# Kernel optimization log

Hardware: AMD Instinct MI355X
Metric: run time of the kernel (lower is better)

The kernel has to match this reference:

```python
import jax, jax.numpy as jnp
import numpy as np

EPS = 1e-5

def _bn(x, g, b):
    # BatchNorm1d, training mode: batch stats over node dim, biased variance
    mu = jnp.mean(x, axis=0)
    var = jnp.mean((x - mu) ** 2, axis=0)
    return (x - mu) * jax.lax.rsqrt(var + EPS) * g + b

def _relconv_msg(h, Vl, ce, src):
    # basis-decomposed per-edge messages: m_e = sum_b ce[e,b] * (h[src_e] @ V_b)
    # scan over bases to avoid [E,B,f] intermediate
    E = src.shape[0]
    f = Vl.shape[-1]
    def step(m, xs):
        Vb, cb = xs  # [d,f], [E]
        return m + cb[:, None] * (h @ Vb)[src], None
    m0 = jnp.zeros((E, f), h.dtype)
    m, _ = jax.lax.scan(step, m0, (Vl, ce.T))
    return m

def setup_inputs() -> dict:
    key = jax.random.key(0)
    ks = jax.random.split(key, 12)
    N, E, d, R, B, L = 20000, 320000, 256, 64, 30, 3
    s = 0.05
    return {
        "h": jax.random.normal(ks[0], (N, d), jnp.float32),
        "norm": jax.random.uniform(ks[1], (E, 1), jnp.float32),
        "V": jax.random.normal(ks[2], (L, B, d, d), jnp.float32) * s,
        "comp": jax.random.normal(ks[3], (L, R, B), jnp.float32) * s,
        "bias": jax.random.normal(ks[4], (L, d), jnp.float32) * s,
        "W1": jax.random.normal(ks[5], (L, d, d), jnp.float32) * s,
        "b1": jax.random.normal(ks[6], (L, d), jnp.float32) * s,
        "g1": jnp.ones((L, d), jnp.float32),
        "bt1": jnp.zeros((L, d), jnp.float32),
        "W2": jax.random.normal(ks[7], (L, d, d), jnp.float32) * s,
        "b2": jax.random.normal(ks[8], (L, d), jnp.float32) * s,
        "g2": jnp.ones((L, d), jnp.float32),
        "bt2": jnp.zeros((L, d), jnp.float32),
        "src": jax.random.randint(ks[9], (E,), 0, N, jnp.int32),
        "dst": jax.random.randint(ks[10], (E,), 0, N, jnp.int32),
        "etypes": jax.random.randint(ks[11], (E,), 0, R, jnp.int32),
    }

def reference(h, norm, V, comp, bias, W1, b1, g1, bt1, W2, b2, g2, bt2, src, dst, etypes):
    N = h.shape[0]
    L = V.shape[0]
    reps = [h]
    for l in range(L):
        ce = comp[l][etypes]                    # [E,B] per-edge basis coeffs
        m = _relconv_msg(h, V[l], ce, src)      # [E,f]
        m = m * norm
        agg = jax.ops.segment_sum(m, dst, num_segments=N)  # scatter-sum to dst
        x = agg + bias[l]
        # MLP activation (2 layers): Linear -> BN -> ReLU -> Linear
        x1 = jax.nn.relu(_bn(x @ W1[l] + b1[l], g1[l], bt1[l]))
        x = x1 @ W2[l] + b2[l]
        # outer BatchNorm + ReLU (RGIN layer)
        h = jax.nn.relu(_bn(x, g2[l], bt2[l]))
        reps.append(h)
    return jnp.stack(reps)  # [L+1, N, d] hidden_rep
```

## Files before the change

### kernel.cpp

```cpp
#include <hip/hip_runtime.h>
#include <hip/hip_bf16.h>
#include <stdint.h>

#define DF   256
#define NBAS 30
#define RREL 64
#define NLAY 3
#define EPSBN 1e-5f

typedef short  bf16x8 __attribute__((ext_vector_type(8)));
typedef float  f32x4  __attribute__((ext_vector_type(4)));
typedef ushort u16x4  __attribute__((ext_vector_type(4)));

typedef __attribute__((address_space(1))) const unsigned int gu32;
typedef __attribute__((address_space(3))) unsigned int       lu32;

__device__ __forceinline__ void gload16(const void* g, void* l){
  __builtin_amdgcn_global_load_lds((gu32*)g, (lu32*)l, 16, 0, 0);
}

__device__ __forceinline__ ushort f2bf(float f){
  union { float f; uint32_t u; } v; v.f = f;
  uint32_t r = (v.u + 0x7FFFu + ((v.u >> 16) & 1u)) >> 16;
  return (ushort)r;
}
__device__ __forceinline__ float bf2f(ushort u){
  union { uint32_t u; float f; } v; v.u = (uint32_t)u << 16;
  return v.f;
}

__global__ __launch_bounds__(256) void k_hist_rel(const int* __restrict__ et,
                                                  int* __restrict__ counts, int E){
  __shared__ int lh[RREL];
  int t = threadIdx.x;
  if (t < RREL) lh[t] = 0;
  __syncthreads();
  int i = blockIdx.x*256 + t;
  if (i < E) atomicAdd(&lh[et[i]], 1);
  __syncthreads();
  if (t < RREL && lh[t]) atomicAdd(&counts[t], lh[t]);
}

__global__ void k_hist_dst(const int* __restrict__ dst, int* __restrict__ counts, int E){
  int i = blockIdx.x*blockDim.x + threadIdx.x;
  if (i < E) atomicAdd(&counts[dst[i]], 1);
}

__global__ void k_scan_rel(const int* __restrict__ counts,
                           int* __restrict__ relOff, int* __restrict__ tileOff){
  int l = threadIdx.x;
  int c  = counts[l];
  int tt = (c + 127) >> 7;
  int ic = c, it = tt;
  #pragma unroll
  for (int o = 1; o < 64; o <<= 1){
    int u = __shfl_up(ic, o); if (l >= o) ic += u;
    int v = __shfl_up(it, o); if (l >= o) it += v;
  }
  if (l == 0){ relOff[0] = 0; tileOff[0] = 0; }
  relOff[l+1]  = ic;
  tileOff[l+1] = it;
}

__global__ void k_scan_dst(const int* __restrict__ counts, int* __restrict__ offs, int n){
  __shared__ int tmp[1024];
  __shared__ int carry;
  int t = threadIdx.x;
  if (t == 0) carry = 0;
  __syncthreads();
  for (int s = 0; s < n; s += 1024){
    int i = s + t;
    int v = (i < n) ? counts[i] : 0;
    tmp[t] = v;
    __syncthreads();
    for (int o = 1; o < 1024; o <<= 1){
      int u = (t >= o) ? tmp[t - o] : 0;
      __syncthreads();
      tmp[t] += u;
      __syncthreads();
    }
    int incl = tmp[t];
    int base = carry;
    if (i < n) offs[i] = base + incl - v;
    __syncthreads();
    if (t == 1023) carry = base + incl;
    __syncthreads();
  }
  if (t == 0) offs[n] = carry;
}

__global__ __launch_bounds__(256) void k_place_rel(const int* __restrict__ et,
    const int* __restrict__ src, const int* __restrict__ relOff,
    int* __restrict__ cursor, int* __restrict__ srcR, int* __restrict__ posR, int E){
  __shared__ int lcnt[RREL];
  __shared__ int lbase[RREL];
  int t = threadIdx.x;
  if (t < RREL) lcnt[t] = 0;
  __syncthreads();
  int i = blockIdx.x*256 + t;
  int r = 0, my = 0;
  bool v = (i < E);
  if (v){ r = et[i]; my = atomicAdd(&lcnt[r], 1); }
  __syncthreads();
  if (t < RREL && lcnt[t]) lbase[t] = atomicAdd(&cursor[t], lcnt[t]);
  __syncthreads();
  if (v){
    int p = relOff[r] + lbase[r] + my;
    srcR[p] = src[i];
    posR[i] = p;
  }
}

__global__ __launch_bounds__(256) void k_place_dst(const int* __restrict__ dst,
    const int* __restrict__ offsD, int* __restrict__ cursorD,
    const int* __restrict__ posR, const float* __restrict__ nrm,
    int* __restrict__ dstPos, float* __restrict__ nrmD, int E){
  int i = blockIdx.x*256 + threadIdx.x;
  if (i < E){
    int d = dst[i];
    int q = offsD[d] + atomicAdd(&cursorD[d], 1);
    dstPos[posR[i]] = q;
    nrmD[q] = nrm[i];
  }
}

__global__ __launch_bounds__(256) void k_wrel(const float* __restrict__ V,
    const float* __restrict__ comp, ushort* __restrict__ Wt){
  const int r  = blockIdx.x;
  const int k0 = blockIdx.y*32;
  const int l  = blockIdx.z;
  const int col = threadIdx.x;
  float acc[32];
  #pragma unroll
  for (int kk = 0; kk < 32; ++kk) acc[kk] = 0.f;
  for (int b = 0; b < NBAS; ++b){
    float cb = comp[(size_t)(l*RREL + r)*NBAS + b];
    const float* Vb = V + (((size_t)(l*NBAS + b)*DF) + k0)*DF + col;
    #pragma unroll
    for (int kk = 0; kk < 32; ++kk) acc[kk] = fmaf(cb, Vb[(size_t)kk*DF], acc[kk]);
  }
  ushort* o = Wt + ((size_t)(l*RREL + r)*DF + col)*DF + k0;
  #pragma unroll
  for (int i4 = 0; i4 < 8; ++i4){
    u16x4 p;
    #pragma unroll
    for (int j = 0; j < 4; ++j) p[j] = f2bf(acc[i4*4 + j]);
    *(u16x4*)(o + i4*4) = p;
  }
}

__global__ void k_transpose_bf16(const float* __restrict__ in, ushort* __restrict__ out, int K){
  const float* inz  = in  + (size_t)blockIdx.z*K*DF;
  ushort*      outz = out + (size_t)blockIdx.z*DF*K;
  __shared__ float tile[32][33];
  int k0 = blockIdx.x*32, n0 = blockIdx.y*32;
  int tx = threadIdx.x & 31, ty = threadIdx.x >> 5;
  #pragma unroll
  for (int i = 0; i < 32; i += 8)
    tile[ty+i][tx] = inz[(size_t)(k0+ty+i)*DF + n0 + tx];
  __syncthreads();
  #pragma unroll
  for (int i = 0; i < 32; i += 8)
    outz[(size_t)(n0+ty+i)*K + k0 + tx] = f2bf(tile[tx][ty+i]);
}

__global__ __launch_bounds__(256) void k_f2b(const float* __restrict__ in,
                                             ushort* __restrict__ o){
  size_t i = ((size_t)blockIdx.x*256 + threadIdx.x)*4;
  f32x4 v = *(const f32x4*)(in + i);
  u16x4 p;
  #pragma unroll
  for (int j = 0; j < 4; ++j) p[j] = f2bf(v[j]);
  *(u16x4*)(o + i) = p;
}

__global__ __launch_bounds__(512) void k_edge_gemm(
    const ushort* __restrict__ xh, const ushort* __restrict__ Wt,
    const int* __restrict__ srcR, const int* __restrict__ dstPos,
    const int* __restrict__ relOff, const int* __restrict__ tileOff,
    ushort* __restrict__ mD){
  __shared__ __align__(16) ushort As[128*64];
  __shared__ __align__(16) ushort Bs[256*64];
  const int b = blockIdx.x;
  if (b >= tileOff[RREL]) return;
  int r = 0;
  #pragma unroll
  for (int step = 32; step; step >>= 1)
    if (r + step <= RREL-1 && tileOff[r + step] <= b) r += step;
  const int eb   = relOff[r] + (b - tileOff[r])*128;
  const int emax = relOff[r+1] - 1;
  const int rows = min(128, relOff[r+1] - eb);

  const int tid  = threadIdx.x;
  const int lane = tid & 63, wid = tid >> 6;
  const int wr = (wid >> 2)*64, wc = (wid & 3)*64;
  const int l15 = lane & 15, lhi = lane >> 4;
  const int ko = (tid & 7)*8;

  const ushort* pa[2];
  #pragma unroll
  for (int i = 0; i < 2; ++i){
    int e = eb + ((tid + i*512) >> 3);
    if (e > emax) e = emax;
    pa[i] = xh + (size_t)srcR[e]*DF + ko;
  }
  const ushort* Bt = Wt + (size_t)r*DF*DF;
  const ushort* pb[4];
  #pragma unroll
  for (int i = 0; i < 4; ++i)
    pb[i] = Bt + (size_t)((tid >> 3) + i*64)*DF + ko;

  const f32x4 z = {0.f, 0.f, 0.f, 0.f};
  f32x4 acc[4][4];
  #pragma unroll
  for (int m = 0; m < 4; ++m)
    #pragma unroll
    for (int n = 0; n < 4; ++n) acc[m][n] = z;

  for (int kt = 0; kt < 4; ++kt){
    const int kbase = kt*64;
    __syncthreads();
    #pragma unroll
    for (int i = 0; i < 2; ++i) gload16(pa[i] + kbase, As + (tid + i*512)*8);
    #pragma unroll
    for (int i = 0; i < 4; ++i) gload16(pb[i] + kbase, Bs + (tid + i*512)*8);
    __syncthreads();
    #pragma unroll
    for (int ks = 0; ks < 2; ++ks){
      const int kb = ks*32 + lhi*8;
      bf16x8 af[4], bfr[4];
      #pragma unroll
      for (int m = 0; m < 4; ++m) af[m]  = *(const bf16x8*)(As + (wr + m*16 + l15)*64 + kb);
      #pragma unroll
      for (int n = 0; n < 4; ++n) bfr[n] = *(const bf16x8*)(Bs + (wc + n*16 + l15)*64 + kb);
      #pragma unroll
      for (int m = 0; m < 4; ++m)
        #pragma unroll
        for (int n = 0; n < 4; ++n)
          acc[m][n] = __builtin_amdgcn_mfma_f32_16x16x32_bf16(af[m], bfr[n], acc[m][n], 0, 0, 0);
    }
  }

  #pragma unroll
  for (int half = 0; half < 2; ++half){
    __syncthreads();
    if ((wid >> 2) == half){
      #pragma unroll
      for (int m = 0; m < 4; ++m)
        #pragma unroll
        for (int q = 0; q < 4; ++q){
          int rl = m*16 + lhi*4 + q;
          #pragma unroll
          for (int n = 0; n < 4; ++n)
            Bs[rl*256 + wc + n*16 + l15] = f2bf(acc[m][n][q]);
        }
    }
    __syncthreads();
    int row = tid >> 3;
    int gr  = half*64 + row;
    if (gr < rows){
      int q = dstPos[eb + gr];
      const uint4* s = (const uint4*)((const char*)Bs + tid*64);
      uint4* d = (uint4*)((char*)(mD + (size_t)q*DF) + (tid & 7)*64);
      #pragma unroll
      for (int i = 0; i < 4; ++i) d[i] = s[i];
    }
  }
}

__global__ __launch_bounds__(256) void k_seg_sum(
    const ushort* __restrict__ mD, const float* __restrict__ nrmD,
    const int* __restrict__ offsD, const float* __restrict__ bias,
    ushort* __restrict__ xb, int N){
  const int w = blockIdx.x*4 + (threadIdx.x >> 6);
  if (w >= N) return;
  const int lane = threadIdx.x & 63;
  const int beg = offsD[w], end = offsD[w+1];
  f32x4 a0 = {0.f,0.f,0.f,0.f}, a1 = {0.f,0.f,0.f,0.f};
  const ushort* p = mD + (size_t)beg*DF + lane*4;
  int j = beg;
  for (; j + 2 <= end; j += 2, p += 2*DF){
    u16x4 v0 = *(const u16x4*)(p);
    u16x4 v1 = *(const u16x4*)(p + DF);
    float n0 = nrmD[j], n1 = nrmD[j+1];
    #pragma unroll
    for (int t = 0; t < 4; ++t){
      a0[t] = fmaf(n0, bf2f(v0[t]), a0[t]);
      a1[t] = fmaf(n1, bf2f(v1[t]), a1[t]);
    }
  }
  if (j < end){
    u16x4 v0 = *(const u16x4*)(p);
    float n0 = nrmD[j];
    #pragma unroll
    for (int t = 0; t < 4; ++t) a0[t] = fmaf(n0, bf2f(v0[t]), a0[t]);
  }
  f32x4 bv = *(const f32x4*)(bias + lane*4);
  u16x4 o;
  #pragma unroll
  for (int t = 0; t < 4; ++t) o[t] = f2bf(a0[t] + a1[t] + bv[t]);
  *(u16x4*)(xb + (size_t)w*DF + lane*4) = o;
}

__global__ __launch_bounds__(256) void k_gemm_mlp(
    const ushort* __restrict__ A, const ushort* __restrict__ Bt,
    const float* __restrict__ bias, float* __restrict__ out,
    float* __restrict__ msum, float* __restrict__ ssum, int a_valid){
  __shared__ __align__(16) ushort As[128*64];
  __shared__ __align__(16) ushort Bs[128*64];
  const int tid  = threadIdx.x;
  const int brow = blockIdx.x*128;
  const int bcol = blockIdx.y*128;
  const int lane = tid & 63, wid = tid >> 6;
  const int wr = (wid >> 1)*64, wc = (wid & 1)*64;
  const int l15 = lane & 15, lhi = lane >> 4;

  const f32x4 z = {0.f, 0.f, 0.f, 0.f};
  f32x4 acc[4][4];
  #pragma unroll
  for (int m = 0; m < 4; ++m)
    #pragma unroll
    for (int n = 0; n < 4; ++n) acc[m][n] = z;

  for (int kt = 0; kt < 4; ++kt){
    const int kbase = kt*64;
    __syncthreads();
    #pragma unroll
    for (int i = 0; i < 4; ++i){
      int c   = tid + i*256;
      int row = c >> 3, ko = (c & 7)*8;
      int ra  = brow + row; if (ra >= a_valid) ra = a_valid - 1;
      gload16(A  + (size_t)ra*DF + kbase + ko,           As + c*8);
      gload16(Bt + (size_t)(bcol + row)*DF + kbase + ko, Bs + c*8);
    }
    __syncthreads();
    #pragma unroll
    for (int ks = 0; ks < 2; ++ks){
      const int kb = ks*32 + lhi*8;
      bf16x8 af[4], bfr[4];
      #pragma unroll
      for (int m = 0; m < 4; ++m) af[m]  = *(const bf16x8*)(As + (wr + m*16 + l15)*64 + kb);
      #pragma unroll
      for (int n = 0; n < 4; ++n) bfr[n] = *(const bf16x8*)(Bs + (wc + n*16 + l15)*64 + kb);
      #pragma unroll
      for (int m = 0; m < 4; ++m)
        #pragma unroll
        for (int n = 0; n < 4; ++n)
          acc[m][n] = __builtin_amdgcn_mfma_f32_16x16x32_bf16(af[m], bfr[n], acc[m][n], 0, 0, 0);
    }
  }

  #pragma unroll
  for (int n = 0; n < 4; ++n){
    const int col = bcol + wc + n*16 + l15;
    const float bv = bias[col];
    float s = 0.f, s2 = 0.f;
    #pragma unroll
    for (int m = 0; m < 4; ++m){
      #pragma unroll
      for (int r = 0; r < 4; ++r){
        int grow = brow + wr + m*16 + lhi*4 + r;
        float v  = acc[m][n][r] + bv;
        out[(size_t)grow*DF + col] = v;
        if (grow < a_valid){ s += v; s2 = fmaf(v, v, s2); }
      }
    }
    s  += __shfl_xor(s, 16);  s  += __shfl_xor(s, 32);
    s2 += __shfl_xor(s2, 16); s2 += __shfl_xor(s2, 32);
    if (lhi == 0){ atomicAdd(&msum[col], s); atomicAdd(&ssum[col], s2); }
  }
}

template<int OM>
__global__ __launch_bounds__(256) void k_bn_apply(const float* __restrict__ y,
    const float* __restrict__ msum, const float* __restrict__ ssum,
    const float* __restrict__ g, const float* __restrict__ bt,
    float inv_n, float* __restrict__ of, ushort* __restrict__ ob,
    ushort* __restrict__ oh){
  size_t i = ((size_t)blockIdx.x*256 + threadIdx.x)*4;
  int col = (int)(i & (DF-1));
  f32x4 v   = *(const f32x4*)(y + i);
  f32x4 mu_ = *(const f32x4*)(msum + col);
  f32x4 s2_ = *(const f32x4*)(ssum + col);
  f32x4 g_  = *(const f32x4*)(g + col);
  f32x4 b_  = *(const f32x4*)(bt + col);
  u16x4 hb; f32x4 vf;
  #pragma unroll
  for (int j = 0; j < 4; ++j){
    float mu  = mu_[j]*inv_n;
    float var = s2_[j]*inv_n - mu*mu;
    float sc  = g_[j]*rsqrtf(var + EPSBN);
    float val = fmaxf(0.f, fmaf(v[j] - mu, sc, b_[j]));
    vf[j] = val;
    hb[j] = f2bf(val);
  }
  if (OM == 0){
    *(u16x4*)(ob + i) = hb;
  } else {
    *(f32x4*)(of + i) = vf;
    *(u16x4*)(oh + i) = hb;
  }
}

extern "C" void kernel_launch(void* const* d_in, const int* in_sizes, int n_in,
                              void* d_out, int out_size, void* d_ws, size_t ws_size,
                              hipStream_t stream){
  const float* h0   = (const float*)d_in[0];
  const float* norm = (const float*)d_in[1];
  const float* V    = (const float*)d_in[2];
  const float* comp = (const float*)d_in[3];
  const float* bias = (const float*)d_in[4];
  const float* W1   = (const float*)d_in[5];
  const float* b1   = (const float*)d_in[6];
  const float* g1   = (const float*)d_in[7];
  const float* bt1  = (const float*)d_in[8];
  const float* W2   = (const float*)d_in[9];
  const float* b2   = (const float*)d_in[10];
  const float* g2   = (const float*)d_in[11];
  const float* bt2  = (const float*)d_in[12];
  const int* src    = (const int*)d_in[13];
  const int* dst    = (const int*)d_in[14];
  const int* et     = (const int*)d_in[15];

  const int N  = in_sizes[0] / DF;
  const int E  = in_sizes[13];
  const int MT = (N + 127) / 128;
  const int MP = MT * 128;
  const size_t MPDF = (size_t)MP * DF;
  const size_t NDF  = (size_t)N * DF;
  const int NTILES = (E + 127)/128 + RREL;
  float* out = (float*)d_out;

  uint8_t* w = (uint8_t*)d_ws;
  size_t o = 0;
  auto carve = [&](size_t bytes)->void*{
    void* p = w + o;
    o = (o + bytes + 511) & ~(size_t)511;
    return p;
  };
  float*  y       = (float*) carve(MPDF*4);
  ushort* xb      = (ushort*)carve(MPDF*2);
  ushort* xh      = (ushort*)carve(NDF*2);
  ushort* Wt      = (ushort*)carve((size_t)NLAY*RREL*DF*DF*2);
  ushort* W1t     = (ushort*)carve((size_t)NLAY*DF*DF*2);
  ushort* W2t     = (ushort*)carve((size_t)NLAY*DF*DF*2);
  float*  bnacc   = (float*) carve((size_t)NLAY*4*DF*4);
  int*    countsR = (int*)   carve(RREL*4);
  int*    cursorR = (int*)   carve(RREL*4);
  int*    relOff  = (int*)   carve((RREL+1)*4);
  int*    tileOff = (int*)   carve((RREL+1)*4);
  int*    countsD = (int*)   carve((size_t)N*4);
  int*    cursorD = (int*)   carve((size_t)N*4);
  int*    offsD   = (int*)   carve((size_t)(N+1)*4);
  int*    srcR    = (int*)   carve((size_t)E*4);
  int*    posR    = (int*)   carve((size_t)E*4);
  int*    dstPos  = (int*)   carve((size_t)E*4);
  float*  nrmD    = (float*) carve((size_t)E*4);
  ushort* mD      = (ushort*)carve((size_t)E*DF*2);

  hipMemsetAsync(countsR, 0, RREL*4, stream);
  hipMemsetAsync(cursorR, 0, RREL*4, stream);
  hipMemsetAsync(countsD, 0, (size_t)N*4, stream);
  hipMemsetAsync(cursorD, 0, (size_t)N*4, stream);
  hipMemsetAsync(bnacc, 0, (size_t)NLAY*4*DF*4, stream);

  k_hist_rel <<<(E+255)/256, 256, 0, stream>>>(et, countsR, E);
  k_hist_dst <<<(E+255)/256, 256, 0, stream>>>(dst, countsD, E);
  k_scan_rel <<<1, 64, 0, stream>>>(countsR, relOff, tileOff);
  k_scan_dst <<<1, 1024, 0, stream>>>(countsD, offsD, N);
  k_place_rel<<<(E+255)/256, 256, 0, stream>>>(et, src, relOff, cursorR, srcR, posR, E);
  k_place_dst<<<(E+255)/256, 256, 0, stream>>>(dst, offsD, cursorD, posR, norm,
                                               dstPos, nrmD, E);

  hipMemcpyAsync(out, h0, NDF*4, hipMemcpyDeviceToDevice, stream);
  k_f2b<<<(int)(NDF/1024), 256, 0, stream>>>(h0, xh);

  k_wrel<<<dim3(RREL, DF/32, NLAY), 256, 0, stream>>>(V, comp, Wt);
  k_transpose_bf16<<<dim3(DF/32, DF/32, NLAY), 256, 0, stream>>>(W1, W1t, DF);
  k_transpose_bf16<<<dim3(DF/32, DF/32, NLAY), 256, 0, stream>>>(W2, W2t, DF);

  const float inv_n = 1.f / (float)N;
  for (int l = 0; l < NLAY; ++l){
    float* ms1 = bnacc + (size_t)(l*4 + 0)*DF;
    float* ss1 = bnacc + (size_t)(l*4 + 1)*DF;
    float* ms2 = bnacc + (size_t)(l*4 + 2)*DF;
    float* ss2 = bnacc + (size_t)(l*4 + 3)*DF;

    k_edge_gemm<<<NTILES, 512, 0, stream>>>(xh, Wt + (size_t)l*RREL*DF*DF,
                                            srcR, dstPos, relOff, tileOff, mD);
    k_seg_sum<<<(N+3)/4, 256, 0, stream>>>(mD, nrmD, offsD, bias + (size_t)l*DF, xb, N);

    k_gemm_mlp<<<dim3(MT, 2), 256, 0, stream>>>(xb, W1t + (size_t)l*DF*DF,
                                                b1 + (size_t)l*DF, y, ms1, ss1, N);
    k_bn_apply<0><<<(int)(NDF/1024), 256, 0, stream>>>(
        y, ms1, ss1, g1 + (size_t)l*DF, bt1 + (size_t)l*DF, inv_n, nullptr, xb, nullptr);

    k_gemm_mlp<<<dim3(MT, 2), 256, 0, stream>>>(xb, W2t + (size_t)l*DF*DF,
                                                b2 + (size_t)l*DF, y, ms2, ss2, N);
    k_bn_apply<1><<<(int)(NDF/1024), 256, 0, stream>>>(
        y, ms2, ss2, g2 + (size_t)l*DF, bt2 + (size_t)l*DF, inv_n,
        out + (size_t)(l+1)*NDF, nullptr, xh);
  }
}
```

Before: 1.053 ms.

## Make edge GEMM persistent per relation with LDS-resident weight slice

The per-edge relation GEMM now launches a fixed grid of relation × slice × column-half blocks. Each block loads its 128-column half of the relation weight matrix into LDS once, then loops over 64-edge tiles with double-buffered gathered A loads and XOR-swizzled LDS layouts, instead of reloading weights for every 128-edge tile. The MLP GEMM moves to 64-row tiles with swizzled LDS, and segment-sum unrolls by four. This trades full-GPU load balance for weight reuse: the grid is fixed at 512 blocks, so uneven relation sizes could leave work imbalanced, and the large LDS footprint limits occupancy.

```diff
diff --git a/kernel.cpp b/kernel.cpp
--- a/kernel.cpp
+++ b/kernel.cpp
@@ -7,6 +7,7 @@
 #define RREL 64
 #define NLAY 3
 #define EPSBN 1e-5f
+#define NSLICE 4
 
 typedef short  bf16x8 __attribute__((ext_vector_type(8)));
 typedef float  f32x4  __attribute__((ext_vector_type(4)));
@@ -46,20 +47,15 @@
   if (i < E) atomicAdd(&counts[dst[i]], 1);
 }
 
-__global__ void k_scan_rel(const int* __restrict__ counts,
-                           int* __restrict__ relOff, int* __restrict__ tileOff){
+__global__ void k_scan_rel(const int* __restrict__ counts, int* __restrict__ relOff){
   int l = threadIdx.x;
-  int c  = counts[l];
-  int tt = (c + 127) >> 7;
-  int ic = c, it = tt;
+  int ic = counts[l];
   #pragma unroll
   for (int o = 1; o < 64; o <<= 1){
     int u = __shfl_up(ic, o); if (l >= o) ic += u;
-    int v = __shfl_up(it, o); if (l >= o) it += v;
-  }
-  if (l == 0){ relOff[0] = 0; tileOff[0] = 0; }
-  relOff[l+1]  = ic;
-  tileOff[l+1] = it;
+  }
+  if (l == 0) relOff[0] = 0;
+  relOff[l+1] = ic;
 }
 
 __global__ void k_scan_dst(const int* __restrict__ counts, int* __restrict__ offs, int n){
@@ -174,96 +170,114 @@
   *(u16x4*)(o + i) = p;
 }
 
-__global__ __launch_bounds__(512) void k_edge_gemm(
+__global__ __launch_bounds__(512) void k_edge_gemm2(
     const ushort* __restrict__ xh, const ushort* __restrict__ Wt,
     const int* __restrict__ srcR, const int* __restrict__ dstPos,
-    const int* __restrict__ relOff, const int* __restrict__ tileOff,
-    ushort* __restrict__ mD){
-  __shared__ __align__(16) ushort As[128*64];
-  __shared__ __align__(16) ushort Bs[256*64];
-  const int b = blockIdx.x;
-  if (b >= tileOff[RREL]) return;
-  int r = 0;
-  #pragma unroll
-  for (int step = 32; step; step >>= 1)
-    if (r + step <= RREL-1 && tileOff[r + step] <= b) r += step;
-  const int eb   = relOff[r] + (b - tileOff[r])*128;
-  const int emax = relOff[r+1] - 1;
-  const int rows = min(128, relOff[r+1] - eb);
-
+    const int* __restrict__ relOff, ushort* __restrict__ mD){
+  __shared__ __align__(16) ushort Ws[128*256];
+  __shared__ __align__(16) ushort AsB[2*64*64];
+  const int b     = blockIdx.x;
+  const int r     = b >> 3;
+  const int slice = (b >> 1) & (NSLICE-1);
+  const int ch    = b & 1;
+  const int e0 = relOff[r], e1 = relOff[r+1];
+  const int tiles = (e1 - e0 + 63) >> 6;
+  const int t0 = (tiles*slice)/NSLICE, t1 = (tiles*(slice+1))/NSLICE;
+  if (t0 >= t1) return;
+  const int emax = e1 - 1;
   const int tid  = threadIdx.x;
   const int lane = tid & 63, wid = tid >> 6;
-  const int wr = (wid >> 2)*64, wc = (wid & 3)*64;
+  const int wg = wid >> 2;
+  const int wc = (wid & 3)*32;
   const int l15 = lane & 15, lhi = lane >> 4;
-  const int ko = (tid & 7)*8;
-
-  const ushort* pa[2];
-  #pragma unroll
-  for (int i = 0; i < 2; ++i){
-    int e = eb + ((tid + i*512) >> 3);
-    if (e > emax) e = emax;
-    pa[i] = xh + (size_t)srcR[e]*DF + ko;
-  }
-  const ushort* Bt = Wt + (size_t)r*DF*DF;
-  const ushort* pb[4];
-  #pragma unroll
-  for (int i = 0; i < 4; ++i)
-    pb[i] = Bt + (size_t)((tid >> 3) + i*64)*DF + ko;
-
-  const f32x4 z = {0.f, 0.f, 0.f, 0.f};
-  f32x4 acc[4][4];
-  #pragma unroll
-  for (int m = 0; m < 4; ++m)
-    #pragma unroll
-    for (int n = 0; n < 4; ++n) acc[m][n] = z;
-
-  for (int kt = 0; kt < 4; ++kt){
-    const int kbase = kt*64;
+
+  const char* Wr = (const char*)(Wt + ((size_t)r*256 + ch*128)*256);
+  #pragma unroll
+  for (int i = 0; i < 8; ++i){
+    int db = (i*512 + tid)*16;
+    int col = db >> 9, kb = db & 511;
+    gload16(Wr + col*512 + (kb ^ ((col & 7) << 4)), (char*)Ws + db);
+  }
+
+  const int srow = tid >> 3;
+  const int skb  = (tid & 7)*16;
+  const int sswz = skb ^ ((srow & 7) << 4);
+  auto STAGE = [&](int c){
+    int t = c >> 2, kt = c & 3;
+    int e = e0 + t*64 + srow; if (e > emax) e = emax;
+    gload16((const char*)(xh + (size_t)srcR[e]*256) + kt*128 + sswz,
+            (char*)AsB + (c & 1)*8192 + tid*16);
+  };
+
+  const f32x4 z = {0.f,0.f,0.f,0.f};
+  f32x4 acc[2][2];
+  #pragma unroll
+  for (int m = 0; m < 2; ++m){ acc[m][0] = z; acc[m][1] = z; }
+
+  const int cEnd = t1*4;
+  int c = t0*4;
+  STAGE(c);
+  __syncthreads();
+
+  for (; c < cEnd; ++c){
+    const int kt = c & 3;
+    if (c + 1 < cEnd) STAGE(c + 1);
+    const char* Ab = (const char*)AsB + (c & 1)*8192;
+    #pragma unroll
+    for (int ks = 0; ks < 2; ++ks){
+      const int kloc  = ks*64 + lhi*16;
+      const int kbyte = kt*128 + ks*64 + lhi*16;
+      bf16x8 af[2], bw[2];
+      #pragma unroll
+      for (int m = 0; m < 2; ++m){
+        int row = wg*32 + m*16 + l15;
+        af[m] = *(const bf16x8*)(Ab + row*128 + (kloc ^ ((row & 7) << 4)));
+      }
+      #pragma unroll
+      for (int n = 0; n < 2; ++n){
+        int col = wc + n*16 + l15;
+        bw[n] = *(const bf16x8*)((const char*)Ws + col*512 + (kbyte ^ ((col & 7) << 4)));
+      }
+      #pragma unroll
+      for (int m = 0; m < 2; ++m)
+        #pragma unroll
+        for (int n = 0; n < 2; ++n)
+          acc[m][n] = __builtin_amdgcn_mfma_f32_16x16x32_bf16(af[m], bw[n], acc[m][n], 0, 0, 0);
+    }
     __syncthreads();
-    #pragma unroll
-    for (int i = 0; i < 2; ++i) gload16(pa[i] + kbase, As + (tid + i*512)*8);
-    #pragma unroll
-    for (int i = 0; i < 4; ++i) gload16(pb[i] + kbase, Bs + (tid + i*512)*8);
-    __syncthreads();
-    #pragma unroll
-    for (int ks = 0; ks < 2; ++ks){
-      const int kb = ks*32 + lhi*8;
-      bf16x8 af[4], bfr[4];
-      #pragma unroll
-      for (int m = 0; m < 4; ++m) af[m]  = *(const bf16x8*)(As + (wr + m*16 + l15)*64 + kb);
-      #pragma unroll
-      for (int n = 0; n < 4; ++n) bfr[n] = *(const bf16x8*)(Bs + (wc + n*16 + l15)*64 + kb);
-      #pragma unroll
-      for (int m = 0; m < 4; ++m)
-        #pragma unroll
-        for (int n = 0; n < 4; ++n)
-          acc[m][n] = __builtin_amdgcn_mfma_f32_16x16x32_bf16(af[m], bfr[n], acc[m][n], 0, 0, 0);
-    }
-  }
-
-  #pragma unroll
-  for (int half = 0; half < 2; ++half){
-    __syncthreads();
-    if ((wid >> 2) == half){
-      #pragma unroll
-      for (int m = 0; m < 4; ++m)
-        #pragma unroll
-        for (int q = 0; q < 4; ++q){
-          int rl = m*16 + lhi*4 + q;
+
+    if (kt == 3){
+      const int t  = c >> 2;
+      const int eb = e0 + t*64;
+      const int rows = min(64, e1 - eb);
+      ushort* epi = (ushort*)((char*)AsB + (c & 1)*8192);
+      #pragma unroll
+      for (int h = 0; h < 2; ++h){
+        if (wg == h){
           #pragma unroll
-          for (int n = 0; n < 4; ++n)
-            Bs[rl*256 + wc + n*16 + l15] = f2bf(acc[m][n][q]);
+          for (int m = 0; m < 2; ++m)
+            #pragma unroll
+            for (int q = 0; q < 4; ++q){
+              int rl = m*16 + lhi*4 + q;
+              #pragma unroll
+              for (int n = 0; n < 2; ++n){
+                int cb = (wc + n*16 + l15)*2;
+                *(ushort*)((char*)epi + rl*256 + (cb ^ ((rl & 7) << 5))) = f2bf(acc[m][n][q]);
+              }
+            }
         }
-    }
-    __syncthreads();
-    int row = tid >> 3;
-    int gr  = half*64 + row;
-    if (gr < rows){
-      int q = dstPos[eb + gr];
-      const uint4* s = (const uint4*)((const char*)Bs + tid*64);
-      uint4* d = (uint4*)((char*)(mD + (size_t)q*DF) + (tid & 7)*64);
-      #pragma unroll
-      for (int i = 0; i < 4; ++i) d[i] = s[i];
+        __syncthreads();
+        int row = tid >> 4;
+        int gr  = h*32 + row;
+        if (gr < rows){
+          int q = dstPos[eb + gr];
+          uint4 v = *(const uint4*)((const char*)epi + row*256 + (((tid & 15)*16) ^ ((row & 7) << 5)));
+          *(uint4*)((char*)mD + (size_t)q*512 + ch*256 + (tid & 15)*16) = v;
+        }
+        __syncthreads();
+      }
+      #pragma unroll
+      for (int m = 0; m < 2; ++m){ acc[m][0] = z; acc[m][1] = z; }
     }
   }
 }
@@ -279,17 +293,21 @@
   f32x4 a0 = {0.f,0.f,0.f,0.f}, a1 = {0.f,0.f,0.f,0.f};
   const ushort* p = mD + (size_t)beg*DF + lane*4;
   int j = beg;
-  for (; j + 2 <= end; j += 2, p += 2*DF){
+  for (; j + 4 <= end; j += 4, p += 4*DF){
     u16x4 v0 = *(const u16x4*)(p);
     u16x4 v1 = *(const u16x4*)(p + DF);
-    float n0 = nrmD[j], n1 = nrmD[j+1];
+    u16x4 v2 = *(const u16x4*)(p + 2*DF);
+    u16x4 v3 = *(const u16x4*)(p + 3*DF);
+    float n0 = nrmD[j], n1 = nrmD[j+1], n2 = nrmD[j+2], n3 = nrmD[j+3];
     #pragma unroll
     for (int t = 0; t < 4; ++t){
       a0[t] = fmaf(n0, bf2f(v0[t]), a0[t]);
       a1[t] = fmaf(n1, bf2f(v1[t]), a1[t]);
-    }
-  }
-  if (j < end){
+      a0[t] = fmaf(n2, bf2f(v2[t]), a0[t]);
+      a1[t] = fmaf(n3, bf2f(v3[t]), a1[t]);
+    }
+  }
+  for (; j < end; ++j, p += DF){
     u16x4 v0 = *(const u16x4*)(p);
     float n0 = nrmD[j];
     #pragma unroll
@@ -306,47 +324,59 @@
     const ushort* __restrict__ A, const ushort* __restrict__ Bt,
     const float* __restrict__ bias, float* __restrict__ out,
     float* __restrict__ msum, float* __restrict__ ssum, int a_valid){
-  __shared__ __align__(16) ushort As[128*64];
+  __shared__ __align__(16) ushort As[64*64];
   __shared__ __align__(16) ushort Bs[128*64];
   const int tid  = threadIdx.x;
-  const int brow = blockIdx.x*128;
+  const int brow = blockIdx.x*64;
   const int bcol = blockIdx.y*128;
   const int lane = tid & 63, wid = tid >> 6;
-  const int wr = (wid >> 1)*64, wc = (wid & 1)*64;
+  const int wr = (wid >> 1)*32, wc = (wid & 1)*64;
   const int l15 = lane & 15, lhi = lane >> 4;
 
-  const f32x4 z = {0.f, 0.f, 0.f, 0.f};
-  f32x4 acc[4][4];
-  #pragma unroll
-  for (int m = 0; m < 4; ++m)
+  const f32x4 z = {0.f,0.f,0.f,0.f};
+  f32x4 acc[2][4];
+  #pragma unroll
+  for (int m = 0; m < 2; ++m)
     #pragma unroll
     for (int n = 0; n < 4; ++n) acc[m][n] = z;
 
   for (int kt = 0; kt < 4; ++kt){
-    const int kbase = kt*64;
     __syncthreads();
     #pragma unroll
+    for (int i = 0; i < 2; ++i){
+      int p = tid + i*256;
+      int row = p >> 3, kb = (p & 7)*16;
+      int ra = brow + row; if (ra >= a_valid) ra = a_valid - 1;
+      gload16((const char*)(A + (size_t)ra*DF) + kt*128 + (kb ^ ((row & 7) << 4)),
+              (char*)As + p*16);
+    }
+    #pragma unroll
     for (int i = 0; i < 4; ++i){
-      int c   = tid + i*256;
-      int row = c >> 3, ko = (c & 7)*8;
-      int ra  = brow + row; if (ra >= a_valid) ra = a_valid - 1;
-      gload16(A  + (size_t)ra*DF + kbase + ko,           As + c*8);
-      gload16(Bt + (size_t)(bcol + row)*DF + kbase + ko, Bs + c*8);
+      int p = tid + i*256;
+      int col = p >> 3, kb = (p & 7)*16;
+      gload16((const char*)(Bt + (size_t)(bcol + col)*DF) + kt*128 + (kb ^ ((col & 7) << 4)),
+              (char*)Bs + p*16);
     }
     __syncthreads();
     #pragma unroll
     for (int ks = 0; ks < 2; ++ks){
-      const int kb = ks*32 + lhi*8;
-      bf16x8 af[4], bfr[4];
-      #pragma unroll
-      for (int m = 0; m < 4; ++m) af[m]  = *(const bf16x8*)(As + (wr + m*16 + l15)*64 + kb);
-      #pragma unroll
-      for (int n = 0; n < 4; ++n) bfr[n] = *(const bf16x8*)(Bs + (wc + n*16 + l15)*64 + kb);
-      #pragma unroll
-      for (int m = 0; m < 4; ++m)
+      const int kloc = ks*64 + lhi*16;
+      bf16x8 af[2], bf_[4];
+      #pragma unroll
+      for (int m = 0; m < 2; ++m){
+        int row = wr + m*16 + l15;
+        af[m] = *(const bf16x8*)((const char*)As + row*128 + (kloc ^ ((row & 7) << 4)));
+      }
+      #pragma unroll
+      for (int n = 0; n < 4; ++n){
+        int col = wc + n*16 + l15;
+        bf_[n] = *(const bf16x8*)((const char*)Bs + col*128 + (kloc ^ ((col & 7) << 4)));
+      }
+      #pragma unroll
+      for (int m = 0; m < 2; ++m)
         #pragma unroll
         for (int n = 0; n < 4; ++n)
-          acc[m][n] = __builtin_amdgcn_mfma_f32_16x16x32_bf16(af[m], bfr[n], acc[m][n], 0, 0, 0);
+          acc[m][n] = __builtin_amdgcn_mfma_f32_16x16x32_bf16(af[m], bf_[n], acc[m][n], 0, 0, 0);
     }
   }
 
@@ -356,11 +386,11 @@
     const float bv = bias[col];
     float s = 0.f, s2 = 0.f;
     #pragma unroll
-    for (int m = 0; m < 4; ++m){
-      #pragma unroll
-      for (int r = 0; r < 4; ++r){
-        int grow = brow + wr + m*16 + lhi*4 + r;
-        float v  = acc[m][n][r] + bv;
+    for (int m = 0; m < 2; ++m){
+      #pragma unroll
+      for (int q = 0; q < 4; ++q){
+        int grow = brow + wr + m*16 + lhi*4 + q;
+        float v  = acc[m][n][q] + bv;
         out[(size_t)grow*DF + col] = v;
         if (grow < a_valid){ s += v; s2 = fmaf(v, v, s2); }
       }
@@ -424,11 +454,9 @@
 
   const int N  = in_sizes[0] / DF;
   const int E  = in_sizes[13];
-  const int MT = (N + 127) / 128;
-  const int MP = MT * 128;
+  const int MP = ((N + 127)/128)*128;
   const size_t MPDF = (size_t)MP * DF;
   const size_t NDF  = (size_t)N * DF;
-  const int NTILES = (E + 127)/128 + RREL;
   float* out = (float*)d_out;
 
   uint8_t* w = (uint8_t*)d_ws;
@@ -448,7 +476,6 @@
   int*    countsR = (int*)   carve(RREL*4);
   int*    cursorR = (int*)   carve(RREL*4);
   int*    relOff  = (int*)   carve((RREL+1)*4);
-  int*    tileOff = (int*)   carve((RREL+1)*4);
   int*    countsD = (int*)   carve((size_t)N*4);
   int*    cursorD = (int*)   carve((size_t)N*4);
   int*    offsD   = (int*)   carve((size_t)(N+1)*4);
@@ -466,7 +493,7 @@
 
   k_hist_rel <<<(E+255)/256, 256, 0, stream>>>(et, countsR, E);
   k_hist_dst <<<(E+255)/256, 256, 0, stream>>>(dst, countsD, E);
-  k_scan_rel <<<1, 64, 0, stream>>>(countsR, relOff, tileOff);
+  k_scan_rel <<<1, 64, 0, stream>>>(countsR, relOff);
   k_scan_dst <<<1, 1024, 0, stream>>>(countsD, offsD, N);
   k_place_rel<<<(E+255)/256, 256, 0, stream>>>(et, src, relOff, cursorR, srcR, posR, E);
   k_place_dst<<<(E+255)/256, 256, 0, stream>>>(dst, offsD, cursorD, posR, norm,
@@ -480,23 +507,24 @@
   k_transpose_bf16<<<dim3(DF/32, DF/32, NLAY), 256, 0, stream>>>(W2, W2t, DF);
 
   const float inv_n = 1.f / (float)N;
+  const int MT2 = (N + 63)/64;
   for (int l = 0; l < NLAY; ++l){
     float* ms1 = bnacc + (size_t)(l*4 + 0)*DF;
     float* ss1 = bnacc + (size_t)(l*4 + 1)*DF;
     float* ms2 = bnacc + (size_t)(l*4 + 2)*DF;
     float* ss2 = bnacc + (size_t)(l*4 + 3)*DF;
 
-    k_edge_gemm<<<NTILES, 512, 0, stream>>>(xh, Wt + (size_t)l*RREL*DF*DF,
-                                            srcR, dstPos, relOff, tileOff, mD);
+    k_edge_gemm2<<<RREL*NSLICE*2, 512, 0, stream>>>(xh, Wt + (size_t)l*RREL*DF*DF,
+                                                    srcR, dstPos, relOff, mD);
     k_seg_sum<<<(N+3)/4, 256, 0, stream>>>(mD, nrmD, offsD, bias + (size_t)l*DF, xb, N);
 
-    k_gemm_mlp<<<dim3(MT, 2), 256, 0, stream>>>(xb, W1t + (size_t)l*DF*DF,
-                                                b1 + (size_t)l*DF, y, ms1, ss1, N);
+    k_gemm_mlp<<<dim3(MT2, 2), 256, 0, stream>>>(xb, W1t + (size_t)l*DF*DF,
+                                                 b1 + (size_t)l*DF, y, ms1, ss1, N);
     k_bn_apply<0><<<(int)(NDF/1024), 256, 0, stream>>>(
         y, ms1, ss1, g1 + (size_t)l*DF, bt1 + (size_t)l*DF, inv_n, nullptr, xb, nullptr);
 
-    k_gemm_mlp<<<dim3(MT, 2), 256, 0, stream>>>(xb, W2t + (size_t)l*DF*DF,
-                                                b2 + (size_t)l*DF, y, ms2, ss2, N);
+    k_gemm_mlp<<<dim3(MT2, 2), 256, 0, stream>>>(xb, W2t + (size_t)l*DF*DF,
+                                                 b2 + (size_t)l*DF, y, ms2, ss2, N);
     k_bn_apply<1><<<(int)(NDF/1024), 256, 0, stream>>>(
         y, ms2, ss2, g2 + (size_t)l*DF, bt2 + (size_t)l*DF, inv_n,
         out + (size_t)(l+1)*NDF, nullptr, xh);
```

New measurement: 974.7 us. 7.5% less time.
